# Performance work log

Hardware: AMD Instinct MI355X
Metric: run time of the kernel (lower is better)

The kernel has to match this reference:

```python
import jax, jax.numpy as jnp
import numpy as np

N = 200000   # nodes
E = 400000   # edges
G = 4096     # graphs in batch
F_IN = 77    # atom feature dim
D = 128      # dim_drug
L = 3        # layer_drug
BN_EPS = 1e-5


def setup_inputs() -> dict:
    key = jax.random.key(0)
    ks = jax.random.split(key, 16)
    inp = {}
    inp["x"] = jax.random.normal(ks[0], (N, F_IN), jnp.float32)
    inp["edge_index"] = jax.random.randint(ks[1], (2, E), 0, N, dtype=jnp.int64)
    inp["batch"] = jnp.sort(jax.random.randint(ks[2], (N,), 0, G, dtype=jnp.int64))
    dims = [F_IN, D, D]
    i = 3
    for l in range(L):
        din = dims[l]
        inp[f"w1_{l}"] = jax.random.normal(ks[i], (din, D), jnp.float32) / np.sqrt(din); i += 1
        inp[f"b1_{l}"] = jnp.zeros((D,), jnp.float32)
        inp[f"w2_{l}"] = jax.random.normal(ks[i], (D, D), jnp.float32) / np.sqrt(D); i += 1
        inp[f"b2_{l}"] = jnp.zeros((D,), jnp.float32)
        inp[f"gamma_{l}"] = jnp.ones((D,), jnp.float32)
        inp[f"beta_{l}"] = jnp.zeros((D,), jnp.float32)
    inp["w_emb"] = jax.random.normal(ks[i], (L * D, 256), jnp.float32) / np.sqrt(L * D)
    inp["b_emb"] = jnp.zeros((256,), jnp.float32)
    return inp


def _gin_bn_layer(h, src, dst, w1, b1, w2, b2, gamma, beta):
    # GINConv (eps=0): out_i = MLP(x_i + sum_{j->i} x_j)
    agg = jax.ops.segment_sum(h[src], dst, num_segments=N)  # scatter-add aggregation
    h = h + agg
    h = jax.nn.relu(h @ w1 + b1) @ w2 + b2                  # GIN MLP
    h = jax.nn.relu(h)                                       # outer F.relu
    mu = jnp.mean(h, axis=0)
    var = jnp.var(h, axis=0)                                  # biased var (training-mode BN)
    return (h - mu) * jax.lax.rsqrt(var + BN_EPS) * gamma + beta


def reference(x, edge_index, batch,
              w1_0, b1_0, w2_0, b2_0, gamma_0, beta_0,
              w1_1, b1_1, w2_1, b2_1, gamma_1, beta_1,
              w1_2, b1_2, w2_2, b2_2, gamma_2, beta_2,
              w_emb, b_emb):
    src, dst = edge_index[0], edge_index[1]
    layers = [(w1_0, b1_0, w2_0, b2_0, gamma_0, beta_0),
              (w1_1, b1_1, w2_1, b2_1, gamma_1, beta_1),
              (w1_2, b1_2, w2_2, b2_2, gamma_2, beta_2)]
    h = x
    outs = []
    for (w1, b1, w2, b2, g, b) in layers:
        h = _gin_bn_layer(h, src, dst, w1, b1, w2, b2, g, b)
        outs.append(h)
    node_rep = jnp.concatenate(outs, axis=1)                  # JK 'cat' -> [N, L*D]
    pooled = jax.ops.segment_max(node_rep, batch, num_segments=G)  # global_max_pool -> [G, L*D]
    # drug_emb: Linear -> ReLU -> Dropout (identity in eval)
    return jax.nn.relu(pooled @ w_emb + b_emb)
```

## Files before the change

### kernel.cpp

```cpp
#include <hip/hip_runtime.h>
#include <hip/hip_bf16.h>
#include <float.h>

#define NN 200000
#define NE 400000
#define NG 4096
#define FIN 77
#define DD 128
#define BN_EPS 1e-5f
#define NB_SCAN ((NN + 255) / 256)
#define NBLK (NN / 64)
#define WCAP 1024

typedef float f32x4 __attribute__((ext_vector_type(4)));
typedef short s16x8 __attribute__((ext_vector_type(8)));

__device__ __forceinline__ unsigned short f2bf(float x) {
    unsigned b = __float_as_uint(x);
    unsigned r = (b + 0x7FFFu + ((b >> 16) & 1u)) >> 16;
    return (unsigned short)r;
}
__device__ __forceinline__ float bf2f(unsigned short u) {
    return __uint_as_float(((unsigned)u) << 16);
}

__global__ void detect_kernel(const unsigned* eidx, const unsigned* batch, int* flags) {
    if (threadIdx.x == 0 && blockIdx.x == 0) {
        int e64 = 1, b64 = 1;
        for (int i = 0; i < 16; i++) {
            if (eidx[2 * NE - 1 - 2 * i] != 0u) e64 = 0;
            if (batch[NN - 1 - 2 * i] != 0u) b64 = 0;
        }
        flags[0] = e64;
        flags[1] = b64;
    }
}

__device__ __forceinline__ int load_idx(const void* p, int is64, long long i) {
    return is64 ? (int)((const long long*)p)[i] : ((const int*)p)[i];
}

__global__ void graph_starts_kernel(const void* batch, const int* flags, int* start) {
    int g = blockIdx.x * blockDim.x + threadIdx.x;
    if (g > NG) return;
    int is64 = flags[1];
    int lo = 0, hi = NN;
    while (lo < hi) {
        int mid = (lo + hi) >> 1;
        int v = load_idx(batch, is64, mid);
        if (v < g) lo = mid + 1; else hi = mid;
    }
    start[g] = lo;
}

__global__ void count_kernel(const void* __restrict__ eidx, const int* __restrict__ flags,
                             int* __restrict__ deg) {
    int e = blockIdx.x * 256 + threadIdx.x;
    if (e >= NE) return;
    int dst = load_idx(eidx, flags[0], (long long)NE + e);
    atomicAdd(&deg[dst], 1);
}

__global__ void scan1_kernel(const int* __restrict__ deg, int* __restrict__ incl,
                             int* __restrict__ bsum) {
    __shared__ int sh[256];
    int i = blockIdx.x * 256 + threadIdx.x;
    int v = (i < NN) ? deg[i] : 0;
    sh[threadIdx.x] = v;
    __syncthreads();
    for (int off = 1; off < 256; off <<= 1) {
        int t = (threadIdx.x >= off) ? sh[threadIdx.x - off] : 0;
        __syncthreads();
        sh[threadIdx.x] += t;
        __syncthreads();
    }
    if (i < NN) incl[i] = sh[threadIdx.x];
    if (threadIdx.x == 255) bsum[blockIdx.x] = sh[255];
}

__global__ void scan2_kernel(int* __restrict__ bsum) {
    __shared__ int sh[1024];
    int t = threadIdx.x;
    int orig = (t < NB_SCAN) ? bsum[t] : 0;
    sh[t] = orig;
    __syncthreads();
    for (int off = 1; off < 1024; off <<= 1) {
        int v = (t >= off) ? sh[t - off] : 0;
        __syncthreads();
        sh[t] += v;
        __syncthreads();
    }
    if (t < NB_SCAN) bsum[t] = sh[t] - orig;
}

__global__ void scan3_kernel(const int* __restrict__ incl, const int* __restrict__ deg,
                             const int* __restrict__ bsum, int* __restrict__ rowptr,
                             int* __restrict__ cursor) {
    int i = blockIdx.x * 256 + threadIdx.x;
    if (i < NN) {
        int ex = bsum[blockIdx.x] + incl[i] - deg[i];
        rowptr[i] = ex;
        cursor[i] = ex;
    }
    if (i == 0) rowptr[NN] = NE;
}

__global__ void fill_kernel(const void* __restrict__ eidx, const int* __restrict__ flags,
                            int* __restrict__ cursor, int* __restrict__ slots) {
    int e = blockIdx.x * 256 + threadIdx.x;
    if (e >= NE) return;
    int is64 = flags[0];
    int src = load_idx(eidx, is64, e);
    int dst = load_idx(eidx, is64, (long long)NE + e);
    int pos = atomicAdd(&cursor[dst], 1);
    slots[pos] = src;
}

__global__ void xconv_kernel(const float* __restrict__ x, unsigned short* __restrict__ xb) {
    int idx = blockIdx.x * 256 + threadIdx.x;
    int row = idx / 12, c8 = (idx % 12) * 8;
    union { s16x8 v; unsigned short u[8]; } pk;
#pragma unroll
    for (int j = 0; j < 8; j++) {
        int c = c8 + j;
        pk.u[j] = (c < FIN) ? f2bf(x[(long long)row * FIN + c]) : (unsigned short)0;
    }
    *(s16x8*)&xb[(long long)row * 96 + c8] = pk.v;
}

__global__ void wconv_all_kernel(const float* __restrict__ w10, const float* __restrict__ w20,
                                 const float* __restrict__ w11, const float* __restrict__ w21,
                                 const float* __restrict__ w12, const float* __restrict__ w22,
                                 unsigned short* __restrict__ wtb) {
    int l = blockIdx.x >> 6;
    int idx = (blockIdx.x & 63) * 256 + threadIdx.x;
    int c = idx >> 7, k = idx & 127;
    const float* w1 = (l == 0) ? w10 : ((l == 1) ? w11 : w12);
    const float* w2 = (l == 0) ? w20 : ((l == 1) ? w21 : w22);
    int K1 = (l == 0) ? FIN : DD;
    unsigned short* wt1 = wtb + l * 2 * 16384;
    wt1[idx] = f2bf(k < K1 ? w1[k * DD + c] : 0.f);
    wt1[16384 + idx] = f2bf(w2[k * DD + c]);
}

template <int L0>
__global__ __launch_bounds__(512, 8) void fused_layer(
    const unsigned short* __restrict__ src, const float* __restrict__ ss,
    const int* __restrict__ rowptr, const int* __restrict__ slots,
    const unsigned short* __restrict__ wt1, const unsigned short* __restrict__ wt2,
    const float* __restrict__ b1, const float* __restrict__ b2,
    unsigned short* __restrict__ out, float* __restrict__ partials)
{
    __shared__ unsigned short Xs[64 * 128];
    __shared__ int s_lo[65];
    __shared__ int s_win[WCAP];
    constexpr int SK = L0 ? 96 : 128;
    constexpr int KS1 = L0 ? 3 : 4;
    int tid = threadIdx.x;
    int lane = tid & 63;
    int w = tid >> 6;
    int rowBase = blockIdx.x * 64;

    int wb = rowptr[rowBase];
    int wn = rowptr[rowBase + 64] - wb;
    if (tid < 65) s_lo[tid] = rowptr[rowBase + tid];
    int wcap = (wn < WCAP) ? wn : WCAP;
    for (int i = tid; i < wcap; i += 512) s_win[i] = slots[wb + i];
    __syncthreads();

    {
        int rp = tid >> 4;
        int c8 = (tid & 15) * 8;
        float sc[8], sh[8];
        if (!L0) {
#pragma unroll
            for (int j = 0; j < 8; j++) { sc[j] = ss[c8 + j]; sh[j] = ss[DD + c8 + j]; }
        }
        int rA = rp, rB = 32 + rp;
        int griA = rowBase + rA, griB = rowBase + rB;
        bool skip = (L0 && c8 >= 96);
        s16x8 voA = {}, v0A = {}, v1A = {}, voB = {}, v0B = {}, v1B = {};
        int dA = 0, dB = 0, loA = 0, loB = 0, oA = 0, oB = 0;
        float mA0 = 0.f, mA1 = 0.f, mB0 = 0.f, mB1 = 0.f;
        if (!skip) {
            loA = s_lo[rA]; dA = s_lo[rA + 1] - loA; oA = loA - wb;
            loB = s_lo[rB]; dB = s_lo[rB + 1] - loB; oB = loB - wb;
            int iA0 = (dA > 0) ? ((oA < WCAP) ? s_win[oA] : slots[loA]) : griA;
            int iA1 = (dA > 1) ? ((oA + 1 < WCAP) ? s_win[oA + 1] : slots[loA + 1]) : griA;
            int iB0 = (dB > 0) ? ((oB < WCAP) ? s_win[oB] : slots[loB]) : griB;
            int iB1 = (dB > 1) ? ((oB + 1 < WCAP) ? s_win[oB + 1] : slots[loB + 1]) : griB;
            voA = *(const s16x8*)&src[griA * SK + c8];
            v0A = *(const s16x8*)&src[iA0 * SK + c8];
            v1A = *(const s16x8*)&src[iA1 * SK + c8];
            voB = *(const s16x8*)&src[griB * SK + c8];
            v0B = *(const s16x8*)&src[iB0 * SK + c8];
            v1B = *(const s16x8*)&src[iB1 * SK + c8];
            mA0 = (dA > 0) ? 1.f : 0.f; mA1 = (dA > 1) ? 1.f : 0.f;
            mB0 = (dB > 0) ? 1.f : 0.f; mB1 = (dB > 1) ? 1.f : 0.f;
        }
        float aA[8], aB[8];
#pragma unroll
        for (int j = 0; j < 8; j++) {
            aA[j] = bf2f((unsigned short)voA[j]) + mA0 * bf2f((unsigned short)v0A[j])
                                                 + mA1 * bf2f((unsigned short)v1A[j]);
            aB[j] = bf2f((unsigned short)voB[j]) + mB0 * bf2f((unsigned short)v0B[j])
                                                 + mB1 * bf2f((unsigned short)v1B[j]);
        }
        if (!skip) {
            for (int k = 2; k < dA; k++) {
                int kk = oA + k;
                int sid = (kk < WCAP) ? s_win[kk] : slots[loA + k];
                s16x8 vk = *(const s16x8*)&src[sid * SK + c8];
#pragma unroll
                for (int j = 0; j < 8; j++) aA[j] += bf2f((unsigned short)vk[j]);
            }
            for (int k = 2; k < dB; k++) {
                int kk = oB + k;
                int sid = (kk < WCAP) ? s_win[kk] : slots[loB + k];
                s16x8 vk = *(const s16x8*)&src[sid * SK + c8];
#pragma unroll
                for (int j = 0; j < 8; j++) aB[j] += bf2f((unsigned short)vk[j]);
            }
            if (!L0) {
                float cntA = (float)(dA + 1), cntB = (float)(dB + 1);
#pragma unroll
                for (int j = 0; j < 8; j++) {
                    aA[j] = aA[j] * sc[j] + cntA * sh[j];
                    aB[j] = aB[j] * sc[j] + cntB * sh[j];
                }
            }
        } else {
#pragma unroll
            for (int j = 0; j < 8; j++) { aA[j] = 0.f; aB[j] = 0.f; }
        }
        union { s16x8 v; unsigned short u[8]; } pkA, pkB;
#pragma unroll
        for (int j = 0; j < 8; j++) { pkA.u[j] = f2bf(aA[j]); pkB.u[j] = f2bf(aB[j]); }
        *(s16x8*)&Xs[rA * 128 + (c8 ^ ((rA & 7) << 3))] = pkA.v;
        *(s16x8*)&Xs[rB * 128 + (c8 ^ ((rB & 7) << 3))] = pkB.v;
    }

    int colbase = w * 16 + (lane & 15);
    s16x8 w1f[4];
    float bs1;
#pragma unroll
    for (int ks = 0; ks < KS1; ks++)
        w1f[ks] = *(const s16x8*)&wt1[colbase * 128 + ks * 32 + (lane >> 4) * 8];
    bs1 = b1[colbase];

    __syncthreads();

    f32x4 acc[4];
#pragma unroll
    for (int rb = 0; rb < 4; rb++) acc[rb] = 0;
#pragma unroll
    for (int ks = 0; ks < KS1; ks++) {
        int lk = ks * 32 + (lane >> 4) * 8;
        s16x8 af[4];
#pragma unroll
        for (int rb = 0; rb < 4; rb++) {
            int r = rb * 16 + (lane & 15);
            af[rb] = *(const s16x8*)&Xs[r * 128 + (lk ^ ((r & 7) << 3))];
        }
#pragma unroll
        for (int rb = 0; rb < 4; rb++)
            acc[rb] = __builtin_amdgcn_mfma_f32_16x16x32_bf16(af[rb], w1f[ks], acc[rb], 0, 0, 0);
    }

    __syncthreads();

#pragma unroll
    for (int rb = 0; rb < 4; rb++) {
#pragma unroll
        for (int reg = 0; reg < 4; reg++) {
            int row = rb * 16 + (lane >> 4) * 4 + reg;
            float v = fmaxf(acc[rb][reg] + bs1, 0.f);
            Xs[row * 128 + (colbase ^ ((row & 7) << 3))] = f2bf(v);
        }
    }

    s16x8 w2f[4];
    float bs2;
#pragma unroll
    for (int ks = 0; ks < 4; ks++)
        w2f[ks] = *(const s16x8*)&wt2[colbase * 128 + ks * 32 + (lane >> 4) * 8];
    bs2 = b2[colbase];

    __syncthreads();

#pragma unroll
    for (int rb = 0; rb < 4; rb++) acc[rb] = 0;
#pragma unroll
    for (int ks = 0; ks < 4; ks++) {
        int lk = ks * 32 + (lane >> 4) * 8;
        s16x8 af[4];
#pragma unroll
        for (int rb = 0; rb < 4; rb++) {
            int r = rb * 16 + (lane & 15);
            af[rb] = *(const s16x8*)&Xs[r * 128 + (lk ^ ((r & 7) << 3))];
        }
#pragma unroll
        for (int rb = 0; rb < 4; rb++)
            acc[rb] = __builtin_amdgcn_mfma_f32_16x16x32_bf16(af[rb], w2f[ks], acc[rb], 0, 0, 0);
    }

    float ps = 0.f, pq = 0.f;
#pragma unroll
    for (int rb = 0; rb < 4; rb++) {
#pragma unroll
        for (int reg = 0; reg < 4; reg++) {
            int row = rowBase + rb * 16 + (lane >> 4) * 4 + reg;
            float v = fmaxf(acc[rb][reg] + bs2, 0.f);
            unsigned short ub = f2bf(v);
            out[row * DD + colbase] = ub;
            float vb = bf2f(ub);
            ps += vb;
            pq += vb * vb;
        }
    }
    ps += __shfl_xor(ps, 16); ps += __shfl_xor(ps, 32);
    pq += __shfl_xor(pq, 16); pq += __shfl_xor(pq, 32);
    if (lane < 16) {
        partials[(long long)blockIdx.x * 256 + colbase] = ps;
        partials[(long long)blockIdx.x * 256 + 128 + colbase] = pq;
    }
}

__global__ __launch_bounds__(256) void bn_red2_fin_kernel(
    const float* __restrict__ partials, float* __restrict__ sums, int* __restrict__ done,
    const float* __restrict__ gamma, const float* __restrict__ beta, float* __restrict__ ss) {
    float s = 0.f;
    for (int b = blockIdx.x; b < NBLK; b += gridDim.x)
        s += partials[(long long)b * 256 + threadIdx.x];
    atomicAdd(&sums[threadIdx.x], s);
    __threadfence();
    __syncthreads();
    __shared__ int tick;
    if (threadIdx.x == 0) tick = atomicAdd(done, 1);
    __syncthreads();
    if (tick == (int)gridDim.x - 1 && threadIdx.x < 128) {
        int c = threadIdx.x;
        float s0 = atomicAdd(&sums[c], 0.f);
        float s1 = atomicAdd(&sums[DD + c], 0.f);
        float mu = s0 / (float)NN;
        float var = s1 / (float)NN - mu * mu;
        float sc = gamma[c] * rsqrtf(var + BN_EPS);
        ss[c] = sc;
        ss[DD + c] = beta[c] - mu * sc;
    }
}

__global__ __launch_bounds__(256) void pool_kernel(const unsigned short* __restrict__ hm,
                                                   const float* __restrict__ ss,
                                                   const int* __restrict__ start,
                                                   float* __restrict__ pooled, int l) {
    __shared__ float red[16][128];
    int g = blockIdx.x;
    int rp = threadIdx.x >> 4;
    int c8 = (threadIdx.x & 15) * 8;
    int lo = start[g], hi = start[g + 1];
    float sc[8], sh[8];
#pragma unroll
    for (int j = 0; j < 8; j++) { sc[j] = ss[c8 + j]; sh[j] = ss[DD + c8 + j]; }
    float m[8];
#pragma unroll
    for (int j = 0; j < 8; j++) m[j] = -FLT_MAX;
    for (int n = lo + rp; n < hi; n += 16) {
        s16x8 v = *(const s16x8*)&hm[(long long)n * DD + c8];
#pragma unroll
        for (int j = 0; j < 8; j++)
            m[j] = fmaxf(m[j], bf2f((unsigned short)v[j]) * sc[j] + sh[j]);
    }
#pragma unroll
    for (int j = 0; j < 8; j++) red[rp][c8 + j] = m[j];
    __syncthreads();
    if (threadIdx.x < 128) {
        int c = threadIdx.x;
        float mm = red[0][c];
#pragma unroll
        for (int r = 1; r < 16; r++) mm = fmaxf(mm, red[r][c]);
        pooled[(long long)g * (3 * DD) + l * DD + c] = mm;
    }
}

__global__ __launch_bounds__(256) void emb_kernel(const float* __restrict__ pooled,
                                                  const float* __restrict__ w,
                                                  const float* __restrict__ b,
                                                  float* __restrict__ out) {
    __shared__ float pl[8][384];
    int tid = threadIdx.x;
    int g0 = blockIdx.x * 8;
#pragma unroll
    for (int i = 0; i < 12; i++) {
        int idx = tid + i * 256;
        int gg = idx / 384, c = idx % 384;
        pl[gg][c] = pooled[(long long)(g0 + gg) * 384 + c];
    }
    __syncthreads();
    float acc[8];
#pragma unroll
    for (int gg = 0; gg < 8; gg++) acc[gg] = 0.f;
    for (int k = 0; k < 384; k++) {
        float wv = w[k * 256 + tid];
#pragma unroll
        for (int gg = 0; gg < 8; gg++) acc[gg] += pl[gg][k] * wv;
    }
    float bb = b[tid];
#pragma unroll
    for (int gg = 0; gg < 8; gg++)
        out[(long long)(g0 + gg) * 256 + tid] = fmaxf(acc[gg] + bb, 0.f);
}

extern "C" void kernel_launch(void* const* d_in, const int* in_sizes, int n_in,
                              void* d_out, int out_size, void* d_ws, size_t ws_size,
                              hipStream_t stream) {
    const float* x = (const float*)d_in[0];
    const void* eidx = d_in[1];
    const void* batch = d_in[2];
    const float* w1[3] = { (const float*)d_in[3],  (const float*)d_in[9],  (const float*)d_in[15] };
    const float* b1[3] = { (const float*)d_in[4],  (const float*)d_in[10], (const float*)d_in[16] };
    const float* w2[3] = { (const float*)d_in[5],  (const float*)d_in[11], (const float*)d_in[17] };
    const float* b2[3] = { (const float*)d_in[6],  (const float*)d_in[12], (const float*)d_in[18] };
    const float* gm[3] = { (const float*)d_in[7],  (const float*)d_in[13], (const float*)d_in[19] };
    const float* bt[3] = { (const float*)d_in[8],  (const float*)d_in[14], (const float*)d_in[20] };
    const float* w_emb = (const float*)d_in[21];
    const float* b_emb = (const float*)d_in[22];
    float* out = (float*)d_out;

    unsigned short* R1 = (unsigned short*)d_ws;
    unsigned short* R2 = R1 + (size_t)NN * DD;
    float* pooled = (float*)(R2 + (size_t)NN * DD);
    float* partials = pooled + (size_t)NG * 384;
    unsigned short* wtb = (unsigned short*)(partials + (size_t)NBLK * 256);
    float* ss = (float*)(wtb + 6 * 16384);
    float* sums = ss + 3 * 256;
    int* done = (int*)(sums + 3 * 256);
    int* deg = done + 4;
    size_t zbytes = (3 * 256) * sizeof(float) + 4 * sizeof(int) + (size_t)NN * sizeof(int);
    int* incl = deg + NN;
    int* bsum = incl + NN;
    int* rowptr = bsum + NB_SCAN;
    int* cursor = rowptr + NN + 1;
    int* slots = cursor + NN;
    int* start = slots + NE;
    int* flags = start + NG + 1;

    detect_kernel<<<1, 64, 0, stream>>>((const unsigned*)eidx, (const unsigned*)batch, flags);
    graph_starts_kernel<<<(NG + 1 + 255) / 256, 256, 0, stream>>>(batch, flags, start);

    hipMemsetAsync(sums, 0, zbytes, stream);

    count_kernel<<<(NE + 255) / 256, 256, 0, stream>>>(eidx, flags, deg);
    scan1_kernel<<<NB_SCAN, 256, 0, stream>>>(deg, incl, bsum);
    scan2_kernel<<<1, 1024, 0, stream>>>(bsum);
    scan3_kernel<<<NB_SCAN, 256, 0, stream>>>(incl, deg, bsum, rowptr, cursor);
    fill_kernel<<<(NE + 255) / 256, 256, 0, stream>>>(eidx, flags, cursor, slots);

    xconv_kernel<<<(NN * 12) / 256, 256, 0, stream>>>(x, R1);
    wconv_all_kernel<<<192, 256, 0, stream>>>(w1[0], w2[0], w1[1], w2[1], w1[2], w2[2], wtb);

    unsigned short* hin[3] = { R1, R2, R1 };
    unsigned short* hout[3] = { R2, R1, R2 };
    for (int l = 0; l < 3; l++) {
        const unsigned short* wt1 = wtb + l * 2 * 16384;
        const unsigned short* wt2 = wt1 + 16384;
        const float* ss_prev = ss + (l - 1) * 256;
        float* ss_l = ss + l * 256;
        if (l == 0)
            fused_layer<1><<<NBLK, 512, 0, stream>>>(hin[l], nullptr, rowptr, slots, wt1, wt2,
                                                     b1[l], b2[l], hout[l], partials);
        else
            fused_layer<0><<<NBLK, 512, 0, stream>>>(hin[l], ss_prev, rowptr, slots, wt1, wt2,
                                                     b1[l], b2[l], hout[l], partials);
        bn_red2_fin_kernel<<<256, 256, 0, stream>>>(partials, sums + l * 256, done + l,
                                                    gm[l], bt[l], ss_l);
        pool_kernel<<<NG, 256, 0, stream>>>(hout[l], ss_l, start, pooled, l);
    }
    emb_kernel<<<NG / 8, 256, 0, stream>>>(pooled, w_emb, b_emb, out);
}
```

Baseline: 371.5 us.

## Merge preprocessing launches and fuse BN finalize with max pooling

Several small setup kernels are merged into one block-indexed launch: x/weight bf16 conversion, zeroing of the scratch buffers (replacing the memset) and index-width detection. Graph-start search and degree counting become a second merged launch. Per layer, the BN-statistics reduction and global max pool are fused into one 256-block kernel. A last-block ticket plus a spin-wait flag acts as a grid barrier, after which each block pools 16 graphs. This removes many launches and inter-kernel gaps, but the pool now runs on 256 blocks instead of 4096. It also relies on all 256 blocks being co-resident for the spin barrier.

```diff
diff --git a/kernel.cpp b/kernel.cpp
--- a/kernel.cpp
+++ b/kernel.cpp
@@ -12,8 +12,14 @@
 #define NBLK (NN / 64)
 #define WCAP 1024
 
+#define XCONV_BLKS (NN * 12 / 256)
+#define WCONV_BLKS 192
+#define ZERO_WORDS16 50194
+#define ZERO_BLKS ((ZERO_WORDS16 + 255) / 256)
+
 typedef float f32x4 __attribute__((ext_vector_type(4)));
 typedef short s16x8 __attribute__((ext_vector_type(8)));
+typedef unsigned int u32x4 __attribute__((ext_vector_type(4)));
 
 __device__ __forceinline__ unsigned short f2bf(float x) {
     unsigned b = __float_as_uint(x);
@@ -24,41 +30,81 @@
     return __uint_as_float(((unsigned)u) << 16);
 }
 
-__global__ void detect_kernel(const unsigned* eidx, const unsigned* batch, int* flags) {
-    if (threadIdx.x == 0 && blockIdx.x == 0) {
-        int e64 = 1, b64 = 1;
-        for (int i = 0; i < 16; i++) {
-            if (eidx[2 * NE - 1 - 2 * i] != 0u) e64 = 0;
-            if (batch[NN - 1 - 2 * i] != 0u) b64 = 0;
-        }
-        flags[0] = e64;
-        flags[1] = b64;
-    }
-}
-
 __device__ __forceinline__ int load_idx(const void* p, int is64, long long i) {
     return is64 ? (int)((const long long*)p)[i] : ((const int*)p)[i];
 }
 
-__global__ void graph_starts_kernel(const void* batch, const int* flags, int* start) {
-    int g = blockIdx.x * blockDim.x + threadIdx.x;
-    if (g > NG) return;
-    int is64 = flags[1];
-    int lo = 0, hi = NN;
-    while (lo < hi) {
-        int mid = (lo + hi) >> 1;
-        int v = load_idx(batch, is64, mid);
-        if (v < g) lo = mid + 1; else hi = mid;
-    }
-    start[g] = lo;
-}
-
-__global__ void count_kernel(const void* __restrict__ eidx, const int* __restrict__ flags,
-                             int* __restrict__ deg) {
-    int e = blockIdx.x * 256 + threadIdx.x;
-    if (e >= NE) return;
-    int dst = load_idx(eidx, flags[0], (long long)NE + e);
-    atomicAdd(&deg[dst], 1);
+__global__ __launch_bounds__(256) void prep_kernel(
+    const float* __restrict__ x, unsigned short* __restrict__ xb,
+    const float* __restrict__ w10, const float* __restrict__ w20,
+    const float* __restrict__ w11, const float* __restrict__ w21,
+    const float* __restrict__ w12, const float* __restrict__ w22,
+    unsigned short* __restrict__ wtb,
+    unsigned int* __restrict__ zbase,
+    const unsigned* __restrict__ eidx, const unsigned* __restrict__ batch,
+    int* __restrict__ flags)
+{
+    int b = blockIdx.x;
+    if (b < XCONV_BLKS) {
+        int idx = b * 256 + threadIdx.x;
+        int row = idx / 12, c8 = (idx % 12) * 8;
+        union { s16x8 v; unsigned short u[8]; } pk;
+#pragma unroll
+        for (int j = 0; j < 8; j++) {
+            int c = c8 + j;
+            pk.u[j] = (c < FIN) ? f2bf(x[(long long)row * FIN + c]) : (unsigned short)0;
+        }
+        *(s16x8*)&xb[(long long)row * 96 + c8] = pk.v;
+    } else if (b < XCONV_BLKS + WCONV_BLKS) {
+        int bb = b - XCONV_BLKS;
+        int l = bb >> 6;
+        int idx = (bb & 63) * 256 + threadIdx.x;
+        int c = idx >> 7, k = idx & 127;
+        const float* w1 = (l == 0) ? w10 : ((l == 1) ? w11 : w12);
+        const float* w2 = (l == 0) ? w20 : ((l == 1) ? w21 : w22);
+        int K1 = (l == 0) ? FIN : DD;
+        unsigned short* wt1 = wtb + l * 2 * 16384;
+        wt1[idx] = f2bf(k < K1 ? w1[k * DD + c] : 0.f);
+        wt1[16384 + idx] = f2bf(w2[k * DD + c]);
+    } else if (b < XCONV_BLKS + WCONV_BLKS + ZERO_BLKS) {
+        int idx = (b - XCONV_BLKS - WCONV_BLKS) * 256 + threadIdx.x;
+        if (idx < ZERO_WORDS16) ((u32x4*)zbase)[idx] = (u32x4){0u, 0u, 0u, 0u};
+    } else {
+        if (threadIdx.x == 0) {
+            int e64 = 1, b64 = 1;
+            for (int i = 0; i < 16; i++) {
+                if (eidx[2 * NE - 1 - 2 * i] != 0u) e64 = 0;
+                if (batch[NN - 1 - 2 * i] != 0u) b64 = 0;
+            }
+            flags[0] = e64;
+            flags[1] = b64;
+        }
+    }
+}
+
+#define GS_BLKS 17
+__global__ __launch_bounds__(256) void gs_count_kernel(
+    const void* __restrict__ batch, const void* __restrict__ eidx,
+    const int* __restrict__ flags, int* __restrict__ start, int* __restrict__ deg)
+{
+    int b = blockIdx.x;
+    if (b < GS_BLKS) {
+        int g = b * 256 + threadIdx.x;
+        if (g > NG) return;
+        int is64 = flags[1];
+        int lo = 0, hi = NN;
+        while (lo < hi) {
+            int mid = (lo + hi) >> 1;
+            int v = load_idx(batch, is64, mid);
+            if (v < g) lo = mid + 1; else hi = mid;
+        }
+        start[g] = lo;
+    } else {
+        int e = (b - GS_BLKS) * 256 + threadIdx.x;
+        if (e >= NE) return;
+        int dst = load_idx(eidx, flags[0], (long long)NE + e);
+        atomicAdd(&deg[dst], 1);
+    }
 }
 
 __global__ void scan1_kernel(const int* __restrict__ deg, int* __restrict__ incl,
@@ -114,33 +160,6 @@
     int dst = load_idx(eidx, is64, (long long)NE + e);
     int pos = atomicAdd(&cursor[dst], 1);
     slots[pos] = src;
-}
-
-__global__ void xconv_kernel(const float* __restrict__ x, unsigned short* __restrict__ xb) {
-    int idx = blockIdx.x * 256 + threadIdx.x;
-    int row = idx / 12, c8 = (idx % 12) * 8;
-    union { s16x8 v; unsigned short u[8]; } pk;
-#pragma unroll
-    for (int j = 0; j < 8; j++) {
-        int c = c8 + j;
-        pk.u[j] = (c < FIN) ? f2bf(x[(long long)row * FIN + c]) : (unsigned short)0;
-    }
-    *(s16x8*)&xb[(long long)row * 96 + c8] = pk.v;
-}
-
-__global__ void wconv_all_kernel(const float* __restrict__ w10, const float* __restrict__ w20,
-                                 const float* __restrict__ w11, const float* __restrict__ w21,
-                                 const float* __restrict__ w12, const float* __restrict__ w22,
-                                 unsigned short* __restrict__ wtb) {
-    int l = blockIdx.x >> 6;
-    int idx = (blockIdx.x & 63) * 256 + threadIdx.x;
-    int c = idx >> 7, k = idx & 127;
-    const float* w1 = (l == 0) ? w10 : ((l == 1) ? w11 : w12);
-    const float* w2 = (l == 0) ? w20 : ((l == 1) ? w21 : w22);
-    int K1 = (l == 0) ? FIN : DD;
-    unsigned short* wt1 = wtb + l * 2 * 16384;
-    wt1[idx] = f2bf(k < K1 ? w1[k * DD + c] : 0.f);
-    wt1[16384 + idx] = f2bf(w2[k * DD + c]);
 }
 
 template <int L0>
@@ -326,60 +345,76 @@
     }
 }
 
-__global__ __launch_bounds__(256) void bn_red2_fin_kernel(
-    const float* __restrict__ partials, float* __restrict__ sums, int* __restrict__ done,
-    const float* __restrict__ gamma, const float* __restrict__ beta, float* __restrict__ ss) {
+__global__ __launch_bounds__(256) void bn_pool_kernel(
+    const float* __restrict__ partials, float* __restrict__ sums,
+    int* __restrict__ done, int* __restrict__ done2,
+    const float* __restrict__ gamma, const float* __restrict__ beta,
+    float* __restrict__ ss,
+    const unsigned short* __restrict__ hm, const int* __restrict__ start,
+    float* __restrict__ pooled, int l)
+{
+    __shared__ float red[16][128];
+    __shared__ float lss[256];
+    int tid = threadIdx.x;
+
     float s = 0.f;
     for (int b = blockIdx.x; b < NBLK; b += gridDim.x)
-        s += partials[(long long)b * 256 + threadIdx.x];
-    atomicAdd(&sums[threadIdx.x], s);
+        s += partials[(long long)b * 256 + tid];
+    atomicAdd(&sums[tid], s);
     __threadfence();
     __syncthreads();
     __shared__ int tick;
-    if (threadIdx.x == 0) tick = atomicAdd(done, 1);
-    __syncthreads();
-    if (tick == (int)gridDim.x - 1 && threadIdx.x < 128) {
-        int c = threadIdx.x;
-        float s0 = atomicAdd(&sums[c], 0.f);
-        float s1 = atomicAdd(&sums[DD + c], 0.f);
-        float mu = s0 / (float)NN;
-        float var = s1 / (float)NN - mu * mu;
-        float sc = gamma[c] * rsqrtf(var + BN_EPS);
-        ss[c] = sc;
-        ss[DD + c] = beta[c] - mu * sc;
-    }
-}
-
-__global__ __launch_bounds__(256) void pool_kernel(const unsigned short* __restrict__ hm,
-                                                   const float* __restrict__ ss,
-                                                   const int* __restrict__ start,
-                                                   float* __restrict__ pooled, int l) {
-    __shared__ float red[16][128];
-    int g = blockIdx.x;
-    int rp = threadIdx.x >> 4;
-    int c8 = (threadIdx.x & 15) * 8;
-    int lo = start[g], hi = start[g + 1];
+    if (tid == 0) tick = atomicAdd(done, 1);
+    __syncthreads();
+    if (tick == (int)gridDim.x - 1) {
+        if (tid < 128) {
+            int c = tid;
+            float s0 = atomicAdd(&sums[c], 0.f);
+            float s1 = atomicAdd(&sums[DD + c], 0.f);
+            float mu = s0 / (float)NN;
+            float var = s1 / (float)NN - mu * mu;
+            float sc = gamma[c] * rsqrtf(var + BN_EPS);
+            ss[c] = sc;
+            ss[DD + c] = beta[c] - mu * sc;
+        }
+        __threadfence();
+        __syncthreads();
+        if (tid == 0) atomicExch(done2, 1);
+    }
+    if (tid == 0) {
+        while (atomicAdd(done2, 0) == 0) __builtin_amdgcn_s_sleep(8);
+    }
+    __syncthreads();
+    lss[tid] = atomicAdd(&ss[tid], 0.f);
+    __syncthreads();
+
+    int rp = tid >> 4;
+    int c8 = (tid & 15) * 8;
     float sc[8], sh[8];
 #pragma unroll
-    for (int j = 0; j < 8; j++) { sc[j] = ss[c8 + j]; sh[j] = ss[DD + c8 + j]; }
-    float m[8];
-#pragma unroll
-    for (int j = 0; j < 8; j++) m[j] = -FLT_MAX;
-    for (int n = lo + rp; n < hi; n += 16) {
-        s16x8 v = *(const s16x8*)&hm[(long long)n * DD + c8];
-#pragma unroll
-        for (int j = 0; j < 8; j++)
-            m[j] = fmaxf(m[j], bf2f((unsigned short)v[j]) * sc[j] + sh[j]);
-    }
-#pragma unroll
-    for (int j = 0; j < 8; j++) red[rp][c8 + j] = m[j];
-    __syncthreads();
-    if (threadIdx.x < 128) {
-        int c = threadIdx.x;
-        float mm = red[0][c];
-#pragma unroll
-        for (int r = 1; r < 16; r++) mm = fmaxf(mm, red[r][c]);
-        pooled[(long long)g * (3 * DD) + l * DD + c] = mm;
+    for (int j = 0; j < 8; j++) { sc[j] = lss[c8 + j]; sh[j] = lss[DD + c8 + j]; }
+    for (int gg = 0; gg < 16; gg++) {
+        int g = blockIdx.x * 16 + gg;
+        int lo = start[g], hi = start[g + 1];
+        float m[8];
+#pragma unroll
+        for (int j = 0; j < 8; j++) m[j] = -FLT_MAX;
+        for (int n = lo + rp; n < hi; n += 16) {
+            s16x8 v = *(const s16x8*)&hm[(long long)n * DD + c8];
+#pragma unroll
+            for (int j = 0; j < 8; j++)
+                m[j] = fmaxf(m[j], bf2f((unsigned short)v[j]) * sc[j] + sh[j]);
+        }
+#pragma unroll
+        for (int j = 0; j < 8; j++) red[rp][c8 + j] = m[j];
+        __syncthreads();
+        if (tid < 128) {
+            float mm = red[0][tid];
+#pragma unroll
+            for (int r = 1; r < 16; r++) mm = fmaxf(mm, red[r][tid]);
+            pooled[(long long)g * (3 * DD) + l * DD + tid] = mm;
+        }
+        __syncthreads();
     }
 }
 
@@ -435,8 +470,8 @@
     float* ss = (float*)(wtb + 6 * 16384);
     float* sums = ss + 3 * 256;
     int* done = (int*)(sums + 3 * 256);
-    int* deg = done + 4;
-    size_t zbytes = (3 * 256) * sizeof(float) + 4 * sizeof(int) + (size_t)NN * sizeof(int);
+    int* done2 = done + 4;
+    int* deg = done2 + 4;
     int* incl = deg + NN;
     int* bsum = incl + NN;
     int* rowptr = bsum + NB_SCAN;
@@ -445,19 +480,16 @@
     int* start = slots + NE;
     int* flags = start + NG + 1;
 
-    detect_kernel<<<1, 64, 0, stream>>>((const unsigned*)eidx, (const unsigned*)batch, flags);
-    graph_starts_kernel<<<(NG + 1 + 255) / 256, 256, 0, stream>>>(batch, flags, start);
-
-    hipMemsetAsync(sums, 0, zbytes, stream);
-
-    count_kernel<<<(NE + 255) / 256, 256, 0, stream>>>(eidx, flags, deg);
+    prep_kernel<<<XCONV_BLKS + WCONV_BLKS + ZERO_BLKS + 1, 256, 0, stream>>>(
+        x, R1, w1[0], w2[0], w1[1], w2[1], w1[2], w2[2], wtb,
+        (unsigned int*)sums, (const unsigned*)eidx, (const unsigned*)batch, flags);
+
+    gs_count_kernel<<<GS_BLKS + (NE + 255) / 256, 256, 0, stream>>>(batch, eidx, flags, start, deg);
+
     scan1_kernel<<<NB_SCAN, 256, 0, stream>>>(deg, incl, bsum);
     scan2_kernel<<<1, 1024, 0, stream>>>(bsum);
     scan3_kernel<<<NB_SCAN, 256, 0, stream>>>(incl, deg, bsum, rowptr, cursor);
     fill_kernel<<<(NE + 255) / 256, 256, 0, stream>>>(eidx, flags, cursor, slots);
-
-    xconv_kernel<<<(NN * 12) / 256, 256, 0, stream>>>(x, R1);
-    wconv_all_kernel<<<192, 256, 0, stream>>>(w1[0], w2[0], w1[1], w2[1], w1[2], w2[2], wtb);
 
     unsigned short* hin[3] = { R1, R2, R1 };
     unsigned short* hout[3] = { R2, R1, R2 };
@@ -472,9 +504,8 @@
         else
             fused_layer<0><<<NBLK, 512, 0, stream>>>(hin[l], ss_prev, rowptr, slots, wt1, wt2,
                                                      b1[l], b2[l], hout[l], partials);
-        bn_red2_fin_kernel<<<256, 256, 0, stream>>>(partials, sums + l * 256, done + l,
-                                                    gm[l], bt[l], ss_l);
-        pool_kernel<<<NG, 256, 0, stream>>>(hout[l], ss_l, start, pooled, l);
+        bn_pool_kernel<<<256, 256, 0, stream>>>(partials, sums + l * 256, done + l, done2 + l,
+                                                gm[l], bt[l], ss_l, hout[l], start, pooled, l);
     }
     emb_kernel<<<NG / 8, 256, 0, stream>>>(pooled, w_emb, b_emb, out);
 }
```

Measured after the change: 459.6 us. +23.7%, slower.
